# Kernel tuning notes

Hardware: AMD Instinct MI355X
Metric: run time of the kernel (lower is better)

Reference implementation:

```python
import jax, jax.numpy as jnp
import numpy as np

BETA = 0.95
THRESHOLD = 1.0
ATAN_ALPHA = 2.0  # snntorch default ATan surrogate slope


@jax.custom_vjp
def spike_fn(u):
    # Heaviside spike with ATan surrogate gradient (snntorch default).
    return (u > 0).astype(u.dtype)

def _spike_fwd(u):
    return spike_fn(u), u

def _spike_bwd(u, g):
    grad = (ATAN_ALPHA / 2.0) / (1.0 + (jnp.pi / 2.0 * ATAN_ALPHA * u) ** 2)
    return (g * grad,)

spike_fn.defvjp(_spike_fwd, _spike_bwd)


def setup_inputs() -> dict:
    key = jax.random.key(0)
    k1, k2 = jax.random.split(key)
    x = jax.random.normal(k1, (255, 256, 784), dtype=jnp.float32)
    # Kaiming-ish init for Linear(784, 40, bias=False)
    W = jax.random.normal(k2, (40, 784), dtype=jnp.float32) * (1.0 / np.sqrt(784.0))
    return {"x": x, "W": W}


def reference(x, W):
    # x: [T, B, 784], W: [40, 784]
    B = x.shape[1]
    n_out = W.shape[0]
    mem0 = jnp.zeros((B, n_out), dtype=x.dtype)

    def step(mem, xt):
        cur = xt @ W.T                                  # [B, 40]
        reset = jax.lax.stop_gradient(
            (mem > THRESHOLD).astype(mem.dtype))        # detached, from prev mem
        mem_new = (BETA * mem + cur) * (1.0 - reset)    # zero-reset mechanism
        spk = spike_fn(mem_new - THRESHOLD)
        return mem_new, (spk, mem_new)

    _, (spk_rec, mem_rec) = jax.lax.scan(step, mem0, x)
    return spk_rec, mem_rec  # each [T, B, 40]
```

## Files before the change

### kernel.cpp

```cpp
#include <hip/hip_runtime.h>
#include <hip/hip_bf16.h>

#define T_STEPS 255
#define BATCH 256
#define NIN 784
#define NOUT 40
#define MROWS (T_STEPS * BATCH)
#define TBN (T_STEPS * BATCH * NOUT)
#define BN_CH (BATCH * NOUT)

#define BM 128
#define NCH 25
#define WB_CHUNK 4608
#define EPS_NEAR 2e-4f
#define SCH 30

typedef short bf16x8 __attribute__((ext_vector_type(8)));
typedef float f32x4 __attribute__((ext_vector_type(4)));

__device__ __forceinline__ unsigned short f2bf(float f) {
  unsigned u = __float_as_uint(f);
  u += 0x7fffu + ((u >> 16) & 1u);
  return (unsigned short)(u >> 16);
}
__device__ __forceinline__ float bf2f(unsigned short h) {
  return __uint_as_float(((unsigned)h) << 16);
}

__global__ __launch_bounds__(256) void wsplit_kernel(
    const float* __restrict__ W, unsigned short* __restrict__ Wbg,
    int* __restrict__ count) {
  int i = blockIdx.x * 256 + threadIdx.x;
  if (i == 0) *count = 0;
  if (i >= NCH * WB_CHUNK) return;
  int e = i & 7, l = (i >> 3) & 63, t = (i >> 9) % 3, s = (i / 1536) % 3,
      c = i / 4608;
  int k = c * 32 + (l >> 4) * 8 + e;
  int n = t * 16 + (l & 15);
  float v = (n < NOUT && k < NIN) ? W[n * NIN + k] : 0.f;
  unsigned short h1 = f2bf(v);
  float r1 = v - bf2f(h1);
  unsigned short h2 = f2bf(r1);
  float r2 = r1 - bf2f(h2);
  unsigned short h3 = f2bf(r2);
  Wbg[i] = (s == 0) ? h1 : (s == 1) ? h2 : h3;
}

__global__ __launch_bounds__(256) void lif_gemm_mfma(
    const float* __restrict__ X, const unsigned short* __restrict__ Wbg,
    float* __restrict__ cur) {
  alignas(16) __shared__ float xs0[4096];
  alignas(16) __shared__ float xs1[4096];
  const int tid = threadIdx.x;
  const int m0 = blockIdx.x * BM;
  const int w = tid >> 6, l = tid & 63;
  const int lr = l & 15, lg = l >> 4;

  f32x4 acc[2][3];
#pragma unroll
  for (int st = 0; st < 2; ++st)
#pragma unroll
    for (int t = 0; t < 3; ++t) acc[st][t] = (f32x4){0.f, 0.f, 0.f, 0.f};

  float4 gxA[4], gxB[4];
  bf16x8 BA[9], BB[9];

#define LOADX(C, DST)                                                     \
  do {                                                                    \
    const int k0_ = (C) * 32;                                             \
    _Pragma("unroll")                                                     \
    for (int i = 0; i < 4; ++i) {                                         \
      int S = tid + i * 256;                                              \
      int row = S >> 3;                                                   \
      int c4 = (S & 7) ^ (row & 7);                                       \
      int k = k0_ + c4 * 4;                                               \
      float4 v = make_float4(0.f, 0.f, 0.f, 0.f);                         \
      if (k < NIN)                                                        \
        v = *reinterpret_cast<const float4*>(X + (size_t)(m0 + row) * NIN + k); \
      DST[i] = v;                                                         \
    }                                                                     \
  } while (0)

#define LOADB(C, DST)                                                     \
  do {                                                                    \
    const unsigned short* base_ = Wbg + (size_t)(C) * WB_CHUNK;           \
    _Pragma("unroll")                                                     \
    for (int q = 0; q < 9; ++q)                                           \
      DST[q] = *reinterpret_cast<const bf16x8*>(base_ + (q * 64 + l) * 8); \
  } while (0)

#define WRITEX(BUF, SRC)                                                  \
  do {                                                                    \
    _Pragma("unroll")                                                     \
    for (int i = 0; i < 4; ++i) {                                         \
      int S = tid + i * 256;                                              \
      *reinterpret_cast<float4*>(&(BUF)[S * 4]) = SRC[i];                 \
    }                                                                     \
  } while (0)

#define COMPUTE(BUF, BSET)                                                \
  do {                                                                    \
    _Pragma("unroll")                                                     \
    for (int st = 0; st < 2; ++st) {                                      \
      int row = (w + st * 4) * 16 + lr;                                   \
      int sA = row * 8 + ((lg * 2) ^ (row & 7));                          \
      int sB = row * 8 + ((lg * 2 + 1) ^ (row & 7));                      \
      float4 fa = *reinterpret_cast<float4*>(&(BUF)[sA * 4]);             \
      float4 fb = *reinterpret_cast<float4*>(&(BUF)[sB * 4]);             \
      float f[8] = {fa.x, fa.y, fa.z, fa.w, fb.x, fb.y, fb.z, fb.w};      \
      union U { unsigned d[4]; bf16x8 v; } A1, A2, A3;                    \
      _Pragma("unroll")                                                   \
      for (int d = 0; d < 4; ++d) {                                       \
        float e0 = f[2 * d], e1 = f[2 * d + 1];                           \
        unsigned short h0 = f2bf(e0), h1 = f2bf(e1);                      \
        float r0 = e0 - bf2f(h0), r1 = e1 - bf2f(h1);                     \
        unsigned short g0 = f2bf(r0), g1 = f2bf(r1);                      \
        float s0 = r0 - bf2f(g0), s1 = r1 - bf2f(g1);                     \
        A1.d[d] = (unsigned)h0 | ((unsigned)h1 << 16);                    \
        A2.d[d] = (unsigned)g0 | ((unsigned)g1 << 16);                    \
        A3.d[d] = (unsigned)f2bf(s0) | ((unsigned)f2bf(s1) << 16);        \
      }                                                                   \
      _Pragma("unroll")                                                   \
      for (int t = 0; t < 3; ++t) {                                       \
        acc[st][t] = __builtin_amdgcn_mfma_f32_16x16x32_bf16(A3.v, BSET[0 * 3 + t], acc[st][t], 0, 0, 0); \
        acc[st][t] = __builtin_amdgcn_mfma_f32_16x16x32_bf16(A1.v, BSET[2 * 3 + t], acc[st][t], 0, 0, 0); \
        acc[st][t] = __builtin_amdgcn_mfma_f32_16x16x32_bf16(A2.v, BSET[1 * 3 + t], acc[st][t], 0, 0, 0); \
        acc[st][t] = __builtin_amdgcn_mfma_f32_16x16x32_bf16(A2.v, BSET[0 * 3 + t], acc[st][t], 0, 0, 0); \
        acc[st][t] = __builtin_amdgcn_mfma_f32_16x16x32_bf16(A1.v, BSET[1 * 3 + t], acc[st][t], 0, 0, 0); \
        acc[st][t] = __builtin_amdgcn_mfma_f32_16x16x32_bf16(A1.v, BSET[0 * 3 + t], acc[st][t], 0, 0, 0); \
      }                                                                   \
    }                                                                     \
  } while (0)

  LOADX(0, gxA);
  LOADB(0, BA);
  WRITEX(xs0, gxA);
  LOADX(1, gxB);
  LOADB(1, BB);
  __syncthreads();

  for (int c = 0; c < 24; c += 2) {
    WRITEX(xs1, gxB);
    if (c + 2 < NCH) LOADX(c + 2, gxA);
    COMPUTE(xs0, BA);
    if (c + 2 < NCH) LOADB(c + 2, BA);
    __syncthreads();
    if (c + 2 < NCH) WRITEX(xs0, gxA);
    if (c + 3 < NCH) LOADX(c + 3, gxB);
    COMPUTE(xs1, BB);
    if (c + 3 < NCH) LOADB(c + 3, BB);
    __syncthreads();
  }
  COMPUTE(xs0, BA);
#undef LOADX
#undef LOADB
#undef WRITEX
#undef COMPUTE

#pragma unroll
  for (int st = 0; st < 2; ++st)
#pragma unroll
    for (int t = 0; t < 3; ++t)
#pragma unroll
      for (int r = 0; r < 4; ++r) {
        int col = t * 16 + lr;
        if (col < NOUT) {
          size_t grow = (size_t)m0 + (w + st * 4) * 16 + lg * 4 + r;
          cur[grow * NOUT + col] = acc[st][t][r];
        }
      }
}

__global__ __launch_bounds__(64) void lif_scan_kernel(
    float* __restrict__ spk, float* __restrict__ curmem,
    int* __restrict__ count, int* __restrict__ wlist) {
  const int idx = blockIdx.x * 64 + threadIdx.x;
  float mem = 0.f;
  bool near = false;
  float c[SCH];
#pragma unroll
  for (int i = 0; i < SCH; ++i) c[i] = curmem[(size_t)i * BN_CH + idx];
  for (int ch = 0; ch < 9; ++ch) {
    const int t0 = ch * SCH;
    float nx[SCH];
    if (ch != 8) {
#pragma unroll
      for (int i = 0; i < SCH; ++i) {
        int t = t0 + SCH + i;
        nx[i] = (t < T_STEPS) ? curmem[(size_t)t * BN_CH + idx] : 0.f;
      }
    }
#pragma unroll
    for (int i = 0; i < SCH; ++i) {
      if (t0 + i < T_STEPS) {
        float reset = (mem > 1.0f) ? 1.0f : 0.0f;
        float decay = 0.95f * mem;
        asm volatile("" : "+v"(decay));
        float summ = decay + c[i];
        float mnew = summ * (1.0f - reset);
        near = near || (fabsf(mnew - 1.0f) < EPS_NEAR);
        curmem[(size_t)(t0 + i) * BN_CH + idx] = mnew;
        spk[(size_t)(t0 + i) * BN_CH + idx] = (mnew > 1.0f) ? 1.0f : 0.0f;
        mem = mnew;
      }
    }
    if (ch != 8) {
#pragma unroll
      for (int i = 0; i < SCH; ++i) c[i] = nx[i];
    }
  }
  if (near) {
    int p = atomicAdd(count, 1);
    wlist[p] = idx;
  }
}

__global__ __launch_bounds__(256) void chaindot_kernel(
    const float* __restrict__ X, const float* __restrict__ W,
    const int* __restrict__ count, const int* __restrict__ wlist,
    float* __restrict__ curfix) {
  const int wv0 = blockIdx.x * 4 + (threadIdx.x >> 6);
  const int l = threadIdx.x & 63;
  const int njobs = *count * 32;
  for (int job = wv0; job < njobs; job += 10240) {
    const int f = job >> 5;
    const int tb = (job & 31) * 8;
    const int idx = wlist[f];
    const int b = idx / NOUT, n = idx % NOUT;
    double wreg[13];
#pragma unroll
    for (int j = 0; j < 12; ++j) wreg[j] = (double)W[n * NIN + l + j * 64];
    wreg[12] = (l < 16) ? (double)W[n * NIN + 768 + l] : 0.0;
#pragma unroll
    for (int u = 0; u < 8; ++u) {
      int t = tb + u;
      if (t >= T_STEPS) break;
      const float* xr = X + (size_t)(t * BATCH + b) * NIN;
      double s = 0.0;
#pragma unroll
      for (int j = 0; j < 12; ++j) s = fma((double)xr[l + j * 64], wreg[j], s);
      if (l < 16) s = fma((double)xr[768 + l], wreg[12], s);
#pragma unroll
      for (int off = 32; off; off >>= 1) s += __shfl_xor(s, off);
      if (l == 0) curfix[(size_t)f * T_STEPS + t] = (float)s;
    }
  }
}

__global__ __launch_bounds__(64) void chainscan_kernel(
    float* __restrict__ spk, float* __restrict__ memout,
    const int* __restrict__ count, const int* __restrict__ wlist,
    const float* __restrict__ curfix) {
  const int f = blockIdx.x * 64 + threadIdx.x;
  if (f >= *count) return;
  const int idx = wlist[f];
  const float* cf = curfix + (size_t)f * T_STEPS;
  float mem = 0.f;
  float c[15];
#pragma unroll
  for (int i = 0; i < 15; ++i) c[i] = cf[i];
  for (int ch = 0; ch < 17; ++ch) {
    const int t0 = ch * 15;
    float nx[15];
    if (ch != 16) {
#pragma unroll
      for (int i = 0; i < 15; ++i) nx[i] = cf[t0 + 15 + i];
    }
#pragma unroll
    for (int i = 0; i < 15; ++i) {
      float reset = (mem > 1.0f) ? 1.0f : 0.0f;
      float decay = 0.95f * mem;
      asm volatile("" : "+v"(decay));
      float summ = decay + c[i];
      float mnew = summ * (1.0f - reset);
      spk[(size_t)(t0 + i) * BN_CH + idx] = (mnew > 1.0f) ? 1.0f : 0.0f;
      memout[(size_t)(t0 + i) * BN_CH + idx] = mnew;
      mem = mnew;
    }
    if (ch != 16) {
#pragma unroll
      for (int i = 0; i < 15; ++i) c[i] = nx[i];
    }
  }
}

extern "C" void kernel_launch(void* const* d_in, const int* in_sizes, int n_in,
                              void* d_out, int out_size, void* d_ws,
                              size_t ws_size, hipStream_t stream) {
  (void)in_sizes; (void)n_in; (void)out_size; (void)ws_size;
  const float* X = (const float*)d_in[0];
  const float* W = (const float*)d_in[1];
  float* out = (float*)d_out;
  float* spk = out;
  float* memout = out + TBN;
  char* ws = (char*)d_ws;
  int* count = (int*)ws;
  int* wlist = (int*)(ws + 64);
  unsigned short* Wbg = (unsigned short*)(ws + 41024);
  float* curfix = (float*)(ws + 271424);

  wsplit_kernel<<<(NCH * WB_CHUNK + 255) / 256, 256, 0, stream>>>(W, Wbg,
                                                                  count);
  lif_gemm_mfma<<<MROWS / BM, 256, 0, stream>>>(X, Wbg, memout);
  lif_scan_kernel<<<BN_CH / 64, 64, 0, stream>>>(spk, memout, count, wlist);
  chaindot_kernel<<<2560, 256, 0, stream>>>(X, W, count, wlist, curfix);
  chainscan_kernel<<<BN_CH / 64, 64, 0, stream>>>(spk, memout, count, wlist,
                                                  curfix);
}
```

Before: 107.1 us.

## Accumulate GEMM per chunk in double, tighten near-threshold fixup, fuse fix kernels

The GEMM tile shrinks to 64 rows per block. Each 32-wide K chunk's MFMA partial is now summed into double accumulators, so the fp32 cur values are more accurate. That allows a smaller near-threshold epsilon, so fewer neurons need the fp64 recompute path. The separate chaindot and chainscan kernels become one chainfix kernel, one block per flagged neuron, with an in-LDS current buffer and a serial scan done by one thread. The costs are per-chunk fp64 adds, B reloads that are no longer double-buffered, and fewer MFMA rows per wave.

```diff
diff --git a/kernel.cpp b/kernel.cpp
--- a/kernel.cpp
+++ b/kernel.cpp
@@ -9,10 +9,10 @@
 #define TBN (T_STEPS * BATCH * NOUT)
 #define BN_CH (BATCH * NOUT)
 
-#define BM 128
+#define BM 64
 #define NCH 25
 #define WB_CHUNK 4608
-#define EPS_NEAR 2e-4f
+#define EPS_NEAR 6e-5f
 #define SCH 30
 
 typedef short bf16x8 __attribute__((ext_vector_type(8)));
@@ -49,27 +49,27 @@
 __global__ __launch_bounds__(256) void lif_gemm_mfma(
     const float* __restrict__ X, const unsigned short* __restrict__ Wbg,
     float* __restrict__ cur) {
-  alignas(16) __shared__ float xs0[4096];
-  alignas(16) __shared__ float xs1[4096];
+  alignas(16) __shared__ float xs0[2048];
+  alignas(16) __shared__ float xs1[2048];
   const int tid = threadIdx.x;
   const int m0 = blockIdx.x * BM;
   const int w = tid >> 6, l = tid & 63;
   const int lr = l & 15, lg = l >> 4;
 
-  f32x4 acc[2][3];
-#pragma unroll
-  for (int st = 0; st < 2; ++st)
-#pragma unroll
-    for (int t = 0; t < 3; ++t) acc[st][t] = (f32x4){0.f, 0.f, 0.f, 0.f};
-
-  float4 gxA[4], gxB[4];
-  bf16x8 BA[9], BB[9];
+  double macc[3][4];
+#pragma unroll
+  for (int t = 0; t < 3; ++t)
+#pragma unroll
+    for (int r = 0; r < 4; ++r) macc[t][r] = 0.0;
+
+  float4 gxA[2], gxB[2];
+  bf16x8 B[9];
 
 #define LOADX(C, DST)                                                     \
   do {                                                                    \
     const int k0_ = (C) * 32;                                             \
     _Pragma("unroll")                                                     \
-    for (int i = 0; i < 4; ++i) {                                         \
+    for (int i = 0; i < 2; ++i) {                                         \
       int S = tid + i * 256;                                              \
       int row = S >> 3;                                                   \
       int c4 = (S & 7) ^ (row & 7);                                       \
@@ -81,94 +81,91 @@
     }                                                                     \
   } while (0)
 
-#define LOADB(C, DST)                                                     \
+#define LOADB(C)                                                          \
   do {                                                                    \
     const unsigned short* base_ = Wbg + (size_t)(C) * WB_CHUNK;           \
     _Pragma("unroll")                                                     \
     for (int q = 0; q < 9; ++q)                                           \
-      DST[q] = *reinterpret_cast<const bf16x8*>(base_ + (q * 64 + l) * 8); \
+      B[q] = *reinterpret_cast<const bf16x8*>(base_ + (q * 64 + l) * 8);  \
   } while (0)
 
 #define WRITEX(BUF, SRC)                                                  \
   do {                                                                    \
     _Pragma("unroll")                                                     \
-    for (int i = 0; i < 4; ++i) {                                         \
+    for (int i = 0; i < 2; ++i) {                                         \
       int S = tid + i * 256;                                              \
       *reinterpret_cast<float4*>(&(BUF)[S * 4]) = SRC[i];                 \
     }                                                                     \
   } while (0)
 
-#define COMPUTE(BUF, BSET)                                                \
-  do {                                                                    \
-    _Pragma("unroll")                                                     \
-    for (int st = 0; st < 2; ++st) {                                      \
-      int row = (w + st * 4) * 16 + lr;                                   \
-      int sA = row * 8 + ((lg * 2) ^ (row & 7));                          \
-      int sB = row * 8 + ((lg * 2 + 1) ^ (row & 7));                      \
-      float4 fa = *reinterpret_cast<float4*>(&(BUF)[sA * 4]);             \
-      float4 fb = *reinterpret_cast<float4*>(&(BUF)[sB * 4]);             \
-      float f[8] = {fa.x, fa.y, fa.z, fa.w, fb.x, fb.y, fb.z, fb.w};      \
-      union U { unsigned d[4]; bf16x8 v; } A1, A2, A3;                    \
+#define COMPUTE(BUF)                                                      \
+  do {                                                                    \
+    int row = w * 16 + lr;                                                \
+    int sA = row * 8 + ((lg * 2) ^ (row & 7));                            \
+    int sB = row * 8 + ((lg * 2 + 1) ^ (row & 7));                        \
+    float4 fa = *reinterpret_cast<float4*>(&(BUF)[sA * 4]);               \
+    float4 fb = *reinterpret_cast<float4*>(&(BUF)[sB * 4]);               \
+    float f[8] = {fa.x, fa.y, fa.z, fa.w, fb.x, fb.y, fb.z, fb.w};        \
+    union U { unsigned d[4]; bf16x8 v; } A1, A2, A3;                      \
+    _Pragma("unroll")                                                     \
+    for (int d = 0; d < 4; ++d) {                                         \
+      float e0 = f[2 * d], e1 = f[2 * d + 1];                             \
+      unsigned short h0 = f2bf(e0), h1 = f2bf(e1);                        \
+      float r0 = e0 - bf2f(h0), r1 = e1 - bf2f(h1);                       \
+      unsigned short g0 = f2bf(r0), g1 = f2bf(r1);                        \
+      float s0 = r0 - bf2f(g0), s1 = r1 - bf2f(g1);                       \
+      A1.d[d] = (unsigned)h0 | ((unsigned)h1 << 16);                      \
+      A2.d[d] = (unsigned)g0 | ((unsigned)g1 << 16);                      \
+      A3.d[d] = (unsigned)f2bf(s0) | ((unsigned)f2bf(s1) << 16);          \
+    }                                                                     \
+    _Pragma("unroll")                                                     \
+    for (int t = 0; t < 3; ++t) {                                         \
+      f32x4 acc = (f32x4){0.f, 0.f, 0.f, 0.f};                            \
+      acc = __builtin_amdgcn_mfma_f32_16x16x32_bf16(A3.v, B[0 * 3 + t], acc, 0, 0, 0); \
+      acc = __builtin_amdgcn_mfma_f32_16x16x32_bf16(A1.v, B[2 * 3 + t], acc, 0, 0, 0); \
+      acc = __builtin_amdgcn_mfma_f32_16x16x32_bf16(A2.v, B[1 * 3 + t], acc, 0, 0, 0); \
+      acc = __builtin_amdgcn_mfma_f32_16x16x32_bf16(A2.v, B[0 * 3 + t], acc, 0, 0, 0); \
+      acc = __builtin_amdgcn_mfma_f32_16x16x32_bf16(A1.v, B[1 * 3 + t], acc, 0, 0, 0); \
+      acc = __builtin_amdgcn_mfma_f32_16x16x32_bf16(A1.v, B[0 * 3 + t], acc, 0, 0, 0); \
       _Pragma("unroll")                                                   \
-      for (int d = 0; d < 4; ++d) {                                       \
-        float e0 = f[2 * d], e1 = f[2 * d + 1];                           \
-        unsigned short h0 = f2bf(e0), h1 = f2bf(e1);                      \
-        float r0 = e0 - bf2f(h0), r1 = e1 - bf2f(h1);                     \
-        unsigned short g0 = f2bf(r0), g1 = f2bf(r1);                      \
-        float s0 = r0 - bf2f(g0), s1 = r1 - bf2f(g1);                     \
-        A1.d[d] = (unsigned)h0 | ((unsigned)h1 << 16);                    \
-        A2.d[d] = (unsigned)g0 | ((unsigned)g1 << 16);                    \
-        A3.d[d] = (unsigned)f2bf(s0) | ((unsigned)f2bf(s1) << 16);        \
-      }                                                                   \
-      _Pragma("unroll")                                                   \
-      for (int t = 0; t < 3; ++t) {                                       \
-        acc[st][t] = __builtin_amdgcn_mfma_f32_16x16x32_bf16(A3.v, BSET[0 * 3 + t], acc[st][t], 0, 0, 0); \
-        acc[st][t] = __builtin_amdgcn_mfma_f32_16x16x32_bf16(A1.v, BSET[2 * 3 + t], acc[st][t], 0, 0, 0); \
-        acc[st][t] = __builtin_amdgcn_mfma_f32_16x16x32_bf16(A2.v, BSET[1 * 3 + t], acc[st][t], 0, 0, 0); \
-        acc[st][t] = __builtin_amdgcn_mfma_f32_16x16x32_bf16(A2.v, BSET[0 * 3 + t], acc[st][t], 0, 0, 0); \
-        acc[st][t] = __builtin_amdgcn_mfma_f32_16x16x32_bf16(A1.v, BSET[1 * 3 + t], acc[st][t], 0, 0, 0); \
-        acc[st][t] = __builtin_amdgcn_mfma_f32_16x16x32_bf16(A1.v, BSET[0 * 3 + t], acc[st][t], 0, 0, 0); \
-      }                                                                   \
+      for (int r = 0; r < 4; ++r) macc[t][r] += (double)acc[r];           \
     }                                                                     \
   } while (0)
 
   LOADX(0, gxA);
-  LOADB(0, BA);
   WRITEX(xs0, gxA);
   LOADX(1, gxB);
-  LOADB(1, BB);
   __syncthreads();
 
   for (int c = 0; c < 24; c += 2) {
+    LOADB(c);
     WRITEX(xs1, gxB);
     if (c + 2 < NCH) LOADX(c + 2, gxA);
-    COMPUTE(xs0, BA);
-    if (c + 2 < NCH) LOADB(c + 2, BA);
-    __syncthreads();
+    COMPUTE(xs0);
+    __syncthreads();
+    LOADB(c + 1);
     if (c + 2 < NCH) WRITEX(xs0, gxA);
     if (c + 3 < NCH) LOADX(c + 3, gxB);
-    COMPUTE(xs1, BB);
-    if (c + 3 < NCH) LOADB(c + 3, BB);
-    __syncthreads();
-  }
-  COMPUTE(xs0, BA);
+    COMPUTE(xs1);
+    __syncthreads();
+  }
+  LOADB(24);
+  COMPUTE(xs0);
 #undef LOADX
 #undef LOADB
 #undef WRITEX
 #undef COMPUTE
 
 #pragma unroll
-  for (int st = 0; st < 2; ++st)
-#pragma unroll
-    for (int t = 0; t < 3; ++t)
-#pragma unroll
-      for (int r = 0; r < 4; ++r) {
-        int col = t * 16 + lr;
-        if (col < NOUT) {
-          size_t grow = (size_t)m0 + (w + st * 4) * 16 + lg * 4 + r;
-          cur[grow * NOUT + col] = acc[st][t][r];
-        }
-      }
+  for (int t = 0; t < 3; ++t)
+#pragma unroll
+    for (int r = 0; r < 4; ++r) {
+      int col = t * 16 + lr;
+      if (col < NOUT) {
+        size_t grow = (size_t)m0 + w * 16 + lg * 4 + r;
+        cur[grow * NOUT + col] = (float)macc[t][r];
+      }
+    }
 }
 
 __global__ __launch_bounds__(64) void lif_scan_kernel(
@@ -215,72 +212,51 @@
   }
 }
 
-__global__ __launch_bounds__(256) void chaindot_kernel(
+__global__ __launch_bounds__(256) void chainfix_kernel(
     const float* __restrict__ X, const float* __restrict__ W,
-    const int* __restrict__ count, const int* __restrict__ wlist,
-    float* __restrict__ curfix) {
-  const int wv0 = blockIdx.x * 4 + (threadIdx.x >> 6);
+    float* __restrict__ spk, float* __restrict__ memout,
+    const int* __restrict__ count, const int* __restrict__ wlist) {
+  __shared__ float cf[256];
+  const int nw = threadIdx.x >> 6;
   const int l = threadIdx.x & 63;
-  const int njobs = *count * 32;
-  for (int job = wv0; job < njobs; job += 10240) {
-    const int f = job >> 5;
-    const int tb = (job & 31) * 8;
+  const int nf = *count;
+  for (int f = blockIdx.x; f < nf; f += gridDim.x) {
     const int idx = wlist[f];
     const int b = idx / NOUT, n = idx % NOUT;
     double wreg[13];
 #pragma unroll
     for (int j = 0; j < 12; ++j) wreg[j] = (double)W[n * NIN + l + j * 64];
     wreg[12] = (l < 16) ? (double)W[n * NIN + 768 + l] : 0.0;
-#pragma unroll
-    for (int u = 0; u < 8; ++u) {
-      int t = tb + u;
-      if (t >= T_STEPS) break;
-      const float* xr = X + (size_t)(t * BATCH + b) * NIN;
-      double s = 0.0;
-#pragma unroll
-      for (int j = 0; j < 12; ++j) s = fma((double)xr[l + j * 64], wreg[j], s);
-      if (l < 16) s = fma((double)xr[768 + l], wreg[12], s);
-#pragma unroll
-      for (int off = 32; off; off >>= 1) s += __shfl_xor(s, off);
-      if (l == 0) curfix[(size_t)f * T_STEPS + t] = (float)s;
-    }
-  }
-}
-
-__global__ __launch_bounds__(64) void chainscan_kernel(
-    float* __restrict__ spk, float* __restrict__ memout,
-    const int* __restrict__ count, const int* __restrict__ wlist,
-    const float* __restrict__ curfix) {
-  const int f = blockIdx.x * 64 + threadIdx.x;
-  if (f >= *count) return;
-  const int idx = wlist[f];
-  const float* cf = curfix + (size_t)f * T_STEPS;
-  float mem = 0.f;
-  float c[15];
-#pragma unroll
-  for (int i = 0; i < 15; ++i) c[i] = cf[i];
-  for (int ch = 0; ch < 17; ++ch) {
-    const int t0 = ch * 15;
-    float nx[15];
-    if (ch != 16) {
-#pragma unroll
-      for (int i = 0; i < 15; ++i) nx[i] = cf[t0 + 15 + i];
-    }
-#pragma unroll
-    for (int i = 0; i < 15; ++i) {
-      float reset = (mem > 1.0f) ? 1.0f : 0.0f;
-      float decay = 0.95f * mem;
-      asm volatile("" : "+v"(decay));
-      float summ = decay + c[i];
-      float mnew = summ * (1.0f - reset);
-      spk[(size_t)(t0 + i) * BN_CH + idx] = (mnew > 1.0f) ? 1.0f : 0.0f;
-      memout[(size_t)(t0 + i) * BN_CH + idx] = mnew;
-      mem = mnew;
-    }
-    if (ch != 16) {
-#pragma unroll
-      for (int i = 0; i < 15; ++i) c[i] = nx[i];
-    }
+    for (int u = 0; u < 64; ++u) {
+      int t = nw * 64 + u;
+      if (t < T_STEPS) {
+        const float* xr = X + (size_t)(t * BATCH + b) * NIN;
+        double s = 0.0;
+#pragma unroll
+        for (int j = 0; j < 12; ++j)
+          s = fma((double)xr[l + j * 64], wreg[j], s);
+        if (l < 16) s = fma((double)xr[768 + l], wreg[12], s);
+#pragma unroll
+        for (int off = 32; off; off >>= 1) s += __shfl_xor(s, off);
+        if (l == 0) cf[t] = (float)s;
+      }
+    }
+    __syncthreads();
+    if (threadIdx.x == 0) {
+      float mem = 0.f;
+      for (int t = 0; t < T_STEPS; ++t) {
+        float curf = cf[t];
+        float reset = (mem > 1.0f) ? 1.0f : 0.0f;
+        float decay = 0.95f * mem;
+        asm volatile("" : "+v"(decay));
+        float summ = decay + curf;
+        float mnew = summ * (1.0f - reset);
+        spk[(size_t)t * BN_CH + idx] = (mnew > 1.0f) ? 1.0f : 0.0f;
+        memout[(size_t)t * BN_CH + idx] = mnew;
+        mem = mnew;
+      }
+    }
+    __syncthreads();
   }
 }
 
@@ -297,13 +273,10 @@
   int* count = (int*)ws;
   int* wlist = (int*)(ws + 64);
   unsigned short* Wbg = (unsigned short*)(ws + 41024);
-  float* curfix = (float*)(ws + 271424);
 
   wsplit_kernel<<<(NCH * WB_CHUNK + 255) / 256, 256, 0, stream>>>(W, Wbg,
                                                                   count);
   lif_gemm_mfma<<<MROWS / BM, 256, 0, stream>>>(X, Wbg, memout);
   lif_scan_kernel<<<BN_CH / 64, 64, 0, stream>>>(spk, memout, count, wlist);
-  chaindot_kernel<<<2560, 256, 0, stream>>>(X, W, count, wlist, curfix);
-  chainscan_kernel<<<BN_CH / 64, 64, 0, stream>>>(spk, memout, count, wlist,
-                                                  curfix);
-}
+  chainfix_kernel<<<512, 256, 0, stream>>>(X, W, spk, memout, count, wlist);
+}
```

Result: slower. 144.2 us (+34.7%).

## Accumulate GEMM chunks in double, tighten near-threshold eps, fuse chain fix kernels

Applied to the files above, without the earlier changes.

The MFMA GEMM now sums each k-chunk's six split-bf16 products into a fresh fp32 accumulator and adds it into double-precision per-element accumulators. That makes the current estimate more accurate, which lets the near-threshold epsilon shrink so fewer neurons get flagged for the exact fp64 recompute. The separate chaindot and chainscan kernels are merged into one kernel that computes the fp64 dot products for a flagged neuron into shared memory and then runs the serial scan in a single thread. This removes a launch and the curfix round trip, at the cost of extra double adds and registers in the GEMM and a single-thread serial scan per flagged neuron.

```diff
diff --git a/kernel.cpp b/kernel.cpp
--- a/kernel.cpp
+++ b/kernel.cpp
@@ -12,7 +12,7 @@
 #define BM 128
 #define NCH 25
 #define WB_CHUNK 4608
-#define EPS_NEAR 2e-4f
+#define EPS_NEAR 6e-5f
 #define SCH 30
 
 typedef short bf16x8 __attribute__((ext_vector_type(8)));
@@ -56,11 +56,13 @@
   const int w = tid >> 6, l = tid & 63;
   const int lr = l & 15, lg = l >> 4;
 
-  f32x4 acc[2][3];
+  double macc[2][3][4];
 #pragma unroll
   for (int st = 0; st < 2; ++st)
 #pragma unroll
-    for (int t = 0; t < 3; ++t) acc[st][t] = (f32x4){0.f, 0.f, 0.f, 0.f};
+    for (int t = 0; t < 3; ++t)
+#pragma unroll
+      for (int r = 0; r < 4; ++r) macc[st][t][r] = 0.0;
 
   float4 gxA[4], gxB[4];
   bf16x8 BA[9], BB[9];
@@ -122,12 +124,15 @@
       }                                                                   \
       _Pragma("unroll")                                                   \
       for (int t = 0; t < 3; ++t) {                                       \
-        acc[st][t] = __builtin_amdgcn_mfma_f32_16x16x32_bf16(A3.v, BSET[0 * 3 + t], acc[st][t], 0, 0, 0); \
-        acc[st][t] = __builtin_amdgcn_mfma_f32_16x16x32_bf16(A1.v, BSET[2 * 3 + t], acc[st][t], 0, 0, 0); \
-        acc[st][t] = __builtin_amdgcn_mfma_f32_16x16x32_bf16(A2.v, BSET[1 * 3 + t], acc[st][t], 0, 0, 0); \
-        acc[st][t] = __builtin_amdgcn_mfma_f32_16x16x32_bf16(A2.v, BSET[0 * 3 + t], acc[st][t], 0, 0, 0); \
-        acc[st][t] = __builtin_amdgcn_mfma_f32_16x16x32_bf16(A1.v, BSET[1 * 3 + t], acc[st][t], 0, 0, 0); \
-        acc[st][t] = __builtin_amdgcn_mfma_f32_16x16x32_bf16(A1.v, BSET[0 * 3 + t], acc[st][t], 0, 0, 0); \
+        f32x4 acc = (f32x4){0.f, 0.f, 0.f, 0.f};                          \
+        acc = __builtin_amdgcn_mfma_f32_16x16x32_bf16(A3.v, BSET[0 * 3 + t], acc, 0, 0, 0); \
+        acc = __builtin_amdgcn_mfma_f32_16x16x32_bf16(A1.v, BSET[2 * 3 + t], acc, 0, 0, 0); \
+        acc = __builtin_amdgcn_mfma_f32_16x16x32_bf16(A2.v, BSET[1 * 3 + t], acc, 0, 0, 0); \
+        acc = __builtin_amdgcn_mfma_f32_16x16x32_bf16(A2.v, BSET[0 * 3 + t], acc, 0, 0, 0); \
+        acc = __builtin_amdgcn_mfma_f32_16x16x32_bf16(A1.v, BSET[1 * 3 + t], acc, 0, 0, 0); \
+        acc = __builtin_amdgcn_mfma_f32_16x16x32_bf16(A1.v, BSET[0 * 3 + t], acc, 0, 0, 0); \
+        _Pragma("unroll")                                                 \
+        for (int r = 0; r < 4; ++r) macc[st][t][r] += (double)acc[r];     \
       }                                                                   \
     }                                                                     \
   } while (0)
@@ -166,7 +171,7 @@
         int col = t * 16 + lr;
         if (col < NOUT) {
           size_t grow = (size_t)m0 + (w + st * 4) * 16 + lg * 4 + r;
-          cur[grow * NOUT + col] = acc[st][t][r];
+          cur[grow * NOUT + col] = (float)macc[st][t][r];
         }
       }
 }
@@ -215,72 +220,51 @@
   }
 }
 
-__global__ __launch_bounds__(256) void chaindot_kernel(
+__global__ __launch_bounds__(256) void chainfix_kernel(
     const float* __restrict__ X, const float* __restrict__ W,
-    const int* __restrict__ count, const int* __restrict__ wlist,
-    float* __restrict__ curfix) {
-  const int wv0 = blockIdx.x * 4 + (threadIdx.x >> 6);
+    float* __restrict__ spk, float* __restrict__ memout,
+    const int* __restrict__ count, const int* __restrict__ wlist) {
+  __shared__ float cf[256];
+  const int nw = threadIdx.x >> 6;
   const int l = threadIdx.x & 63;
-  const int njobs = *count * 32;
-  for (int job = wv0; job < njobs; job += 10240) {
-    const int f = job >> 5;
-    const int tb = (job & 31) * 8;
+  const int nf = *count;
+  for (int f = blockIdx.x; f < nf; f += gridDim.x) {
     const int idx = wlist[f];
     const int b = idx / NOUT, n = idx % NOUT;
     double wreg[13];
 #pragma unroll
     for (int j = 0; j < 12; ++j) wreg[j] = (double)W[n * NIN + l + j * 64];
     wreg[12] = (l < 16) ? (double)W[n * NIN + 768 + l] : 0.0;
-#pragma unroll
-    for (int u = 0; u < 8; ++u) {
-      int t = tb + u;
-      if (t >= T_STEPS) break;
-      const float* xr = X + (size_t)(t * BATCH + b) * NIN;
-      double s = 0.0;
-#pragma unroll
-      for (int j = 0; j < 12; ++j) s = fma((double)xr[l + j * 64], wreg[j], s);
-      if (l < 16) s = fma((double)xr[768 + l], wreg[12], s);
-#pragma unroll
-      for (int off = 32; off; off >>= 1) s += __shfl_xor(s, off);
-      if (l == 0) curfix[(size_t)f * T_STEPS + t] = (float)s;
-    }
-  }
-}
-
-__global__ __launch_bounds__(64) void chainscan_kernel(
-    float* __restrict__ spk, float* __restrict__ memout,
-    const int* __restrict__ count, const int* __restrict__ wlist,
-    const float* __restrict__ curfix) {
-  const int f = blockIdx.x * 64 + threadIdx.x;
-  if (f >= *count) return;
-  const int idx = wlist[f];
-  const float* cf = curfix + (size_t)f * T_STEPS;
-  float mem = 0.f;
-  float c[15];
-#pragma unroll
-  for (int i = 0; i < 15; ++i) c[i] = cf[i];
-  for (int ch = 0; ch < 17; ++ch) {
-    const int t0 = ch * 15;
-    float nx[15];
-    if (ch != 16) {
-#pragma unroll
-      for (int i = 0; i < 15; ++i) nx[i] = cf[t0 + 15 + i];
-    }
-#pragma unroll
-    for (int i = 0; i < 15; ++i) {
-      float reset = (mem > 1.0f) ? 1.0f : 0.0f;
-      float decay = 0.95f * mem;
-      asm volatile("" : "+v"(decay));
-      float summ = decay + c[i];
-      float mnew = summ * (1.0f - reset);
-      spk[(size_t)(t0 + i) * BN_CH + idx] = (mnew > 1.0f) ? 1.0f : 0.0f;
-      memout[(size_t)(t0 + i) * BN_CH + idx] = mnew;
-      mem = mnew;
-    }
-    if (ch != 16) {
-#pragma unroll
-      for (int i = 0; i < 15; ++i) c[i] = nx[i];
-    }
+    for (int u = 0; u < 64; ++u) {
+      int t = nw * 64 + u;
+      if (t < T_STEPS) {
+        const float* xr = X + (size_t)(t * BATCH + b) * NIN;
+        double s = 0.0;
+#pragma unroll
+        for (int j = 0; j < 12; ++j)
+          s = fma((double)xr[l + j * 64], wreg[j], s);
+        if (l < 16) s = fma((double)xr[768 + l], wreg[12], s);
+#pragma unroll
+        for (int off = 32; off; off >>= 1) s += __shfl_xor(s, off);
+        if (l == 0) cf[t] = (float)s;
+      }
+    }
+    __syncthreads();
+    if (threadIdx.x == 0) {
+      float mem = 0.f;
+      for (int t = 0; t < T_STEPS; ++t) {
+        float curf = cf[t];
+        float reset = (mem > 1.0f) ? 1.0f : 0.0f;
+        float decay = 0.95f * mem;
+        asm volatile("" : "+v"(decay));
+        float summ = decay + curf;
+        float mnew = summ * (1.0f - reset);
+        spk[(size_t)t * BN_CH + idx] = (mnew > 1.0f) ? 1.0f : 0.0f;
+        memout[(size_t)t * BN_CH + idx] = mnew;
+        mem = mnew;
+      }
+    }
+    __syncthreads();
   }
 }
 
@@ -297,13 +281,10 @@
   int* count = (int*)ws;
   int* wlist = (int*)(ws + 64);
   unsigned short* Wbg = (unsigned short*)(ws + 41024);
-  float* curfix = (float*)(ws + 271424);
 
   wsplit_kernel<<<(NCH * WB_CHUNK + 255) / 256, 256, 0, stream>>>(W, Wbg,
                                                                   count);
   lif_gemm_mfma<<<MROWS / BM, 256, 0, stream>>>(X, Wbg, memout);
   lif_scan_kernel<<<BN_CH / 64, 64, 0, stream>>>(spk, memout, count, wlist);
-  chaindot_kernel<<<2560, 256, 0, stream>>>(X, W, count, wlist, curfix);
-  chainscan_kernel<<<BN_CH / 64, 64, 0, stream>>>(spk, memout, count, wlist,
-                                                  curfix);
-}
+  chainfix_kernel<<<512, 256, 0, stream>>>(X, W, spk, memout, count, wlist);
+}
```

Result: slower. 142.3 us (+32.9%).
